# Performance work log

Measured on AMD Instinct MI355X. Metric: run time of the kernel, lower is better.

## Reference

```python
import jax, jax.numpy as jnp
import numpy as np

MODEL_DIM = 1024
NUM_HEADS = 16
K_DIM = MODEL_DIM // NUM_HEADS


def setup_inputs() -> dict:
    key = jax.random.key(0)
    kx, kw1, kw2 = jax.random.split(key, 3)
    B, L, D = 4, 2048, MODEL_DIM
    x = jax.random.normal(kx, (B, L, D), dtype=jnp.float32)
    # nn.Linear(D, 3D, bias=False): y = x @ W^T; store transposed form [D, 3D]
    scale1 = 1.0 / np.sqrt(D)
    Wqkv = jax.random.uniform(kw1, (D, 3 * D), dtype=jnp.float32, minval=-scale1, maxval=scale1)
    Wout = jax.random.uniform(kw2, (D, D), dtype=jnp.float32, minval=-scale1, maxval=scale1)
    return {"x": x, "Wqkv": Wqkv, "Wout": Wout}


def reference(x, Wqkv, Wout):
    B, L, D = x.shape
    H, Kd = NUM_HEADS, K_DIM
    qkv = x @ Wqkv  # [B, L, 3D]
    q, k, v = jnp.split(qkv, 3, axis=-1)

    def heads(t):  # [B, L, D] -> [B, H, L, Kd]
        return t.reshape(B, L, H, Kd).transpose(0, 2, 1, 3)

    qh, kh, vh = heads(q), heads(k), heads(v)
    scores = jnp.einsum('bhqd,bhkd->bhqk', qh, kh) / jnp.sqrt(jnp.float32(Kd))
    causal = jnp.triu(jnp.ones((L, L), dtype=bool), k=1)  # True above diagonal
    scores = jnp.where(causal, -jnp.inf, scores)
    probs = jax.nn.softmax(scores, axis=-1)
    attended = jnp.einsum('bhqk,bhkd->bhqd', probs, vh)
    concatted = attended.transpose(0, 2, 1, 3).reshape(B, L, D)
    # dropout is identity in eval mode
    return concatted @ Wout
```

## Files before the change

kernel.cpp:

```cpp
#include <hip/hip_runtime.h>

typedef unsigned short u16;
typedef unsigned int   u32;
typedef __bf16   bf16x8 __attribute__((ext_vector_type(8)));
typedef float    f32x4  __attribute__((ext_vector_type(4)));
typedef u16      u16x4  __attribute__((ext_vector_type(4)));
typedef u16      u16x8  __attribute__((ext_vector_type(8)));
typedef u32      u32x2  __attribute__((ext_vector_type(2)));
typedef u32      u32x4  __attribute__((ext_vector_type(4)));

#if __has_builtin(__builtin_amdgcn_exp2f)
#define EXP2(x) __builtin_amdgcn_exp2f(x)
#else
#define EXP2(x) exp2f(x)
#endif

__device__ __forceinline__ u16 f2bf(float f) {
    unsigned u = __float_as_uint(f);
    u += 0x7FFFu + ((u >> 16) & 1u);
    return (u16)(u >> 16);
}

__device__ __forceinline__ u32 pack_bf16(float a, float b) {
#if __has_builtin(__builtin_amdgcn_cvt_pk_bf16_f32)
    typedef __bf16 bf16x2 __attribute__((ext_vector_type(2)));
    bf16x2 r = __builtin_amdgcn_cvt_pk_bf16_f32(a, b);
    return __builtin_bit_cast(u32, r);
#else
    return (u32)f2bf(a) | ((u32)f2bf(b) << 16);
#endif
}

__device__ __forceinline__ void async_copy16(const u16* g, u16* l) {
    __builtin_amdgcn_global_load_lds(
        (const __attribute__((address_space(1))) unsigned*)g,
        (__attribute__((address_space(3))) unsigned*)l, 16, 0, 0);
}

__device__ __forceinline__ bf16x8 lds_frag(const u16* p) {
    return *(const bf16x8*)p;
}

__device__ __forceinline__ void permlane32_swap(u32& a, u32& b) {
    asm("v_permlane32_swap_b32 %0, %1" : "+v"(a), "+v"(b));
}
__device__ __forceinline__ void permlane16_swap(u32& a, u32& b) {
    asm("v_permlane16_swap_b32 %0, %1" : "+v"(a), "+v"(b));
}

__global__ __launch_bounds__(256) void prep(const float* __restrict__ x,
                                            const float* __restrict__ Wqkv,
                                            const float* __restrict__ Wout,
                                            u16* __restrict__ xb,
                                            u16* __restrict__ wqkv_t,
                                            u16* __restrict__ wout_t) {
    __shared__ u16 t[64 * 72];
    const int bid = blockIdx.x;
    const int tid = threadIdx.x;

    if (bid >= 1024) {
        size_t i = ((size_t)(bid - 1024) * 256 + tid) * 8;
        float4 v0 = *(const float4*)(x + i);
        float4 v1 = *(const float4*)(x + i + 4);
        u16x8 o = { f2bf(v0.x), f2bf(v0.y), f2bf(v0.z), f2bf(v0.w),
                    f2bf(v1.x), f2bf(v1.y), f2bf(v1.z), f2bf(v1.w) };
        *(u16x8*)(xb + i) = o;
        return;
    }

    const float* W;  u16* Wt;  int Kd, Nd, n0, k0;
    if (bid < 768) { W = Wqkv; Wt = wqkv_t; Kd = 1024; Nd = 3072;
                     n0 = (bid % 48) * 64; k0 = (bid / 48) * 64; }
    else           { W = Wout; Wt = wout_t; Kd = 1024; Nd = 1024;
                     n0 = ((bid - 768) % 16) * 64; k0 = ((bid - 768) / 16) * 64; }
#pragma unroll
    for (int i = 0; i < 4; ++i) {
        int lin = i * 256 + tid;
        int kr = lin >> 4, nc = (lin & 15) << 2;
        float4 v = *(const float4*)(W + (size_t)(k0 + kr) * Nd + n0 + nc);
        u16x4 o = { f2bf(v.x), f2bf(v.y), f2bf(v.z), f2bf(v.w) };
        *(u16x4*)&t[kr * 72 + nc] = o;
    }
    __syncthreads();
#pragma unroll
    for (int i = 0; i < 2; ++i) {
        int lin = i * 256 + tid;
        int nr = lin >> 3, kc = (lin & 7) << 3;
        u16x8 o;
#pragma unroll
        for (int jj = 0; jj < 8; ++jj) o[jj] = t[(kc + jj) * 72 + nr];
        *(u16x8*)(Wt + (size_t)(n0 + nr) * Kd + k0 + kc) = o;
    }
}

__global__ __launch_bounds__(256) void gemm_qkv(const u16* __restrict__ A,
                                                const u16* __restrict__ Bt,
                                                u16* __restrict__ outb,
                                                int K, int N) {
    __shared__ u16 As[2][128 * 32];
    __shared__ u16 Bs[2][128 * 32];
    const int tid = threadIdx.x;
    const int lane = tid & 63;
    const int wv = tid >> 6;
    const int wr = (wv >> 1) * 64;
    const int wc = (wv & 1) * 64;
    const int qd = lane >> 4;
    const int c  = lane & 15;

    const int flat = blockIdx.x;
    const int r_ = flat & 7;
    const int q_ = flat >> 3;
    const int m0 = ((r_ >> 1) * 16 + q_ / 12) * 128;
    const int n0 = ((r_ & 1) * 12 + q_ % 12) * 128;

    const int srow = tid >> 2;
    const int sg = ((tid & 3) ^ ((srow >> 1) & 3)) << 3;

    const u16* Ag0 = A  + (size_t)(m0 +      srow) * K + sg;
    const u16* Ag1 = A  + (size_t)(m0 + 64 + srow) * K + sg;
    const u16* Bg0 = Bt + (size_t)(n0 +      srow) * K + sg;
    const u16* Bg1 = Bt + (size_t)(n0 + 64 + srow) * K + sg;

    const u32 fsw = (qd ^ ((c >> 1) & 3)) << 3;
    const u32 a_off = (wr + c) * 32 + fsw;
    const u32 b_off = (wc + c) * 32 + fsw;

    f32x4 acc[4][4] = {};

    async_copy16(Ag0, &As[0][tid * 8]);
    async_copy16(Ag1, &As[0][2048 + tid * 8]);
    async_copy16(Bg0, &Bs[0][tid * 8]);
    async_copy16(Bg1, &Bs[0][2048 + tid * 8]);

    int p = 0;
    for (int k0 = 0; k0 < K; k0 += 32) {
        __syncthreads();
        if (k0 + 32 < K) {
            const int np = p ^ 1;
            async_copy16(Ag0 + k0 + 32, &As[np][tid * 8]);
            async_copy16(Ag1 + k0 + 32, &As[np][2048 + tid * 8]);
            async_copy16(Bg0 + k0 + 32, &Bs[np][tid * 8]);
            async_copy16(Bg1 + k0 + 32, &Bs[np][2048 + tid * 8]);
        }
        bf16x8 af[4], bfr[4];
#pragma unroll
        for (int i = 0; i < 4; ++i) af[i]  = lds_frag(&As[p][a_off + i * 512]);
#pragma unroll
        for (int j = 0; j < 4; ++j) bfr[j] = lds_frag(&Bs[p][b_off + j * 512]);
#pragma unroll
        for (int i = 0; i < 4; ++i)
#pragma unroll
            for (int j = 0; j < 4; ++j)
                acc[i][j] = __builtin_amdgcn_mfma_f32_16x16x32_bf16(af[i], bfr[j], acc[i][j], 0, 0, 0);
        p ^= 1;
    }

#pragma unroll
    for (int i = 0; i < 4; ++i)
#pragma unroll
        for (int j = 0; j < 4; ++j) {
            int n = n0 + wc + j * 16 + c;
            int which = n >> 10, h = (n >> 6) & 15, kd = n & 63;
            int m_base = m0 + wr + i * 16 + qd * 4;
            int b = m_base >> 11, l0 = m_base & 2047;
            int bh = b * 16 + h;
            if (which == 2) {
                u32x2 o2;
                o2[0] = pack_bf16(acc[i][j][0], acc[i][j][1]);
                o2[1] = pack_bf16(acc[i][j][2], acc[i][j][3]);
                *(u32x2*)(outb + (size_t)(128 + bh) * 131072 + (size_t)kd * 2048 + l0) = o2;
            } else if (which == 0) {
#pragma unroll
                for (int r = 0; r < 4; ++r)
                    outb[(size_t)bh * 131072 + (size_t)(l0 + r) * 64 + kd] =
                        f2bf(acc[i][j][r] * 0.1803368801f);
            } else {
#pragma unroll
                for (int r = 0; r < 4; ++r)
                    outb[(size_t)(64 + bh) * 131072 + (size_t)(l0 + r) * 64 + kd] =
                        f2bf(acc[i][j][r]);
            }
        }
}

__global__ __launch_bounds__(256) void gemm_out(const u16* __restrict__ A,
                                                const u16* __restrict__ Bt,
                                                float* __restrict__ outf,
                                                int K, int N) {
    __shared__ u16 As[2][64 * 32];
    __shared__ u16 Bs[2][128 * 32];
    const int tid = threadIdx.x;
    const int lane = tid & 63;
    const int wv = tid >> 6;
    const int wr = (wv >> 1) * 32;
    const int wc = (wv & 1) * 64;
    const int qd = lane >> 4;
    const int c  = lane & 15;

    const int flat = blockIdx.x + 8 * blockIdx.y;
    const int r_ = flat & 7;
    const int q_ = flat >> 3;
    const int m0 = (r_ * 16 + (q_ >> 3)) * 64;
    const int n0 = (q_ & 7) * 128;

    const int srow = tid >> 2;
    const int sg = ((tid & 3) ^ ((srow >> 1) & 3)) << 3;

    const u16* Ag0 = A  + (size_t)(m0 +      srow) * K + sg;
    const u16* Bg0 = Bt + (size_t)(n0 +      srow) * K + sg;
    const u16* Bg1 = Bt + (size_t)(n0 + 64 + srow) * K + sg;

    const u32 fsw = (qd ^ ((c >> 1) & 3)) << 3;
    const u32 a_off = (wr + c) * 32 + fsw;
    const u32 b_off = (wc + c) * 32 + fsw;

    f32x4 acc[2][4] = {};

    async_copy16(Ag0, &As[0][tid * 8]);
    async_copy16(Bg0, &Bs[0][tid * 8]);
    async_copy16(Bg1, &Bs[0][2048 + tid * 8]);

    int p = 0;
    for (int k0 = 0; k0 < K; k0 += 32) {
        __syncthreads();
        if (k0 + 32 < K) {
            const int np = p ^ 1;
            async_copy16(Ag0 + k0 + 32, &As[np][tid * 8]);
            async_copy16(Bg0 + k0 + 32, &Bs[np][tid * 8]);
            async_copy16(Bg1 + k0 + 32, &Bs[np][2048 + tid * 8]);
        }
        bf16x8 af[2], bfr[4];
#pragma unroll
        for (int i = 0; i < 2; ++i) af[i]  = lds_frag(&As[p][a_off + i * 512]);
#pragma unroll
        for (int j = 0; j < 4; ++j) bfr[j] = lds_frag(&Bs[p][b_off + j * 512]);
#pragma unroll
        for (int i = 0; i < 2; ++i)
#pragma unroll
            for (int j = 0; j < 4; ++j)
                acc[i][j] = __builtin_amdgcn_mfma_f32_16x16x32_bf16(af[i], bfr[j], acc[i][j], 0, 0, 0);
        p ^= 1;
    }

#pragma unroll
    for (int i = 0; i < 2; ++i)
#pragma unroll
        for (int j = 0; j < 4; ++j)
#pragma unroll
            for (int r = 0; r < 4; ++r) {
                int m = m0 + wr + i * 16 + qd * 4 + r;
                int n = n0 + wc + j * 16 + c;
                outf[(size_t)m * N + n] = acc[i][j][r];
            }
}

#define ATTN_S_AB(KSB)                                                        \
    do {                                                                      \
        _Pragma("unroll") for (int f = 0; f < 8; ++f) {                       \
            sa[f] = f32x4{-8.f, -8.f, -8.f, -8.f};                            \
            sb[f] = f32x4{-8.f, -8.f, -8.f, -8.f};                            \
        }                                                                     \
        __builtin_amdgcn_s_setprio(1);                                        \
        _Pragma("unroll") for (int ks = 0; ks < 2; ++ks) {                    \
            const u16* kp = (KSB) + kf_off[ks];                               \
            _Pragma("unroll") for (int f = 0; f < 8; ++f) {                   \
                bf16x8 kf = lds_frag(kp + f * 1024);                          \
                sa[f] = __builtin_amdgcn_mfma_f32_16x16x32_bf16(              \
                    kf, qa[ks], sa[f], 0, 0, 0);                              \
                sb[f] = __builtin_amdgcn_mfma_f32_16x16x32_bf16(              \
                    kf, qb[ks], sb[f], 0, 0, 0);                              \
            }                                                                 \
        }                                                                     \
        __builtin_amdgcn_s_setprio(0);                                        \
    } while (0)

#define ATTN_FINISH_AB(VTB, KT)                                               \
    do {                                                                      \
        if ((KT) == qt) {                                                     \
            _Pragma("unroll") for (int f = 0; f < 8; ++f)                     \
                _Pragma("unroll") for (int r = 0; r < 4; ++r) {               \
                    int key = (KT) * 128 + f * 16 + qd * 4 + r;               \
                    if (key > qa_row) sa[f][r] = -3e38f;                      \
                    if (key > qb_row) sb[f][r] = -3e38f;                      \
                }                                                             \
        }                                                                     \
        _Pragma("unroll") for (int f = 0; f < 8; ++f) {                       \
            _Pragma("unroll") for (int r = 0; r < 4; ++r) {                   \
                sa[f][r] = EXP2(sa[f][r]);                                    \
                sb[f][r] = EXP2(sb[f][r]);                                    \
            }                                                                 \
            rva += sa[f];                                                     \
            rvb += sb[f];                                                     \
        }                                                                     \
        _Pragma("unroll") for (int kc = 0; kc < 4; ++kc) {                    \
            u32 a0 = pack_bf16(sa[2 * kc][0], sa[2 * kc][1]);                 \
            u32 a1 = pack_bf16(sa[2 * kc + 1][0], sa[2 * kc + 1][1]);         \
            u32 b0 = pack_bf16(sa[2 * kc][2], sa[2 * kc][3]);                 \
            u32 b1 = pack_bf16(sa[2 * kc + 1][2], sa[2 * kc + 1][3]);         \
            permlane32_swap(a0, a1); permlane16_swap(a0, a1);                 \
            permlane32_swap(b0, b1); permlane16_swap(b0, b1);                 \
            u32x4 wpa = {a0, b0, a1, b1};                                     \
            bf16x8 pa = __builtin_bit_cast(bf16x8, wpa);                      \
            u32 c0 = pack_bf16(sb[2 * kc][0], sb[2 * kc][1]);                 \
            u32 c1 = pack_bf16(sb[2 * kc + 1][0], sb[2 * kc + 1][1]);         \
            u32 d0 = pack_bf16(sb[2 * kc][2], sb[2 * kc][3]);                 \
            u32 d1 = pack_bf16(sb[2 * kc + 1][2], sb[2 * kc + 1][3]);         \
            permlane32_swap(c0, c1); permlane16_swap(c0, c1);                 \
            permlane32_swap(d0, d1); permlane16_swap(d0, d1);                 \
            u32x4 wpb = {c0, d0, c1, d1};                                     \
            bf16x8 pb = __builtin_bit_cast(bf16x8, wpb);                      \
            const u16* vp = (VTB) + vf_off[kc];                               \
            __builtin_amdgcn_s_setprio(1);                                    \
            _Pragma("unroll") for (int jo = 0; jo < 4; ++jo) {                \
                bf16x8 vf = lds_frag(vp + jo * 2048);                         \
                acca[jo] = __builtin_amdgcn_mfma_f32_16x16x32_bf16(           \
                    vf, pa, acca[jo], 0, 0, 0);                               \
                accb[jo] = __builtin_amdgcn_mfma_f32_16x16x32_bf16(           \
                    vf, pb, accb[jo], 0, 0, 0);                               \
            }                                                                 \
            __builtin_amdgcn_s_setprio(0);                                    \
        }                                                                     \
    } while (0)

__global__ __launch_bounds__(256, 2) void attn_kernel(const u16* __restrict__ qkv,
                                                      u16* __restrict__ att) {
    __shared__ u16 Ks[2][128 * 64];
    __shared__ u16 Vt[2][64 * 128];

    const int tid = threadIdx.x;
    const int lane = tid & 63;
    const int w = tid >> 6;
    const int qd = lane >> 4;
    const int c = lane & 15;

    const int flat = blockIdx.x + 8 * blockIdx.y;
    const int bh = (flat & 7) + 8 * ((flat >> 3) & 7);
    const int bx = flat >> 6;
    const int b = bh >> 4, h = bh & 15;

    const u16* Qg = qkv + (size_t)bh * 131072;
    const u16* Kg = qkv + (size_t)(64 + bh) * 131072;
    const u16* Vg = qkv + (size_t)(128 + bh) * 131072;

    u32 kf_off[2];
#pragma unroll
    for (int ks = 0; ks < 2; ++ks)
        kf_off[ks] = c * 64 + (((ks * 4 + qd) ^ (c & 7)) << 3);
    u32 vf_off[4];
#pragma unroll
    for (int kc = 0; kc < 4; ++kc)
        vf_off[kc] = c * 128 + (((kc * 4 + qd) ^ c) << 3);

    auto issue_copy = [&](int t, u16* kd, u16* vd) {
#pragma unroll
        for (int it = 0; it < 4; ++it) {
            int lin = it * 256 + tid;
            int krw = lin >> 3, kch = lin & 7;
            int vrw = lin >> 4, vch = lin & 15;
            async_copy16(Kg + (size_t)t * 8192 + krw * 64 + ((kch ^ (krw & 7)) << 3),
                         kd + lin * 8);
            async_copy16(Vg + (size_t)t * 128 + (size_t)vrw * 2048 + ((vch ^ (vrw & 15)) << 3),
                         vd + lin * 8);
        }
    };

#pragma unroll 1
    for (int seg = 0; seg < 2; ++seg) {
        const int qt = seg ? (15 - bx) : bx;
        const int qa_row = qt * 128 + w * 32 + c;
        const int qb_row = qa_row + 16;

        bf16x8 qa[2], qb[2];
#pragma unroll
        for (int ks = 0; ks < 2; ++ks) {
            qa[ks] = *(const bf16x8*)(Qg + (size_t)qa_row * 64 + ks * 32 + qd * 8);
            qb[ks] = *(const bf16x8*)(Qg + (size_t)qb_row * 64 + ks * 32 + qd * 8);
        }

        f32x4 acca[4] = {}, accb[4] = {};
        f32x4 rva = {}, rvb = {};
        f32x4 sa[8], sb[8];

        const int nkt = qt + 1;

        __syncthreads();
        issue_copy(0, Ks[0], Vt[0]);
        __syncthreads();
        if (nkt > 1) issue_copy(1, Ks[1], Vt[1]);

#pragma unroll 1
        for (int kt = 0; kt < nkt; ++kt) {
            const int p = kt & 1;
            ATTN_S_AB(Ks[p]);
            ATTN_FINISH_AB(Vt[p], kt);
            if (kt + 1 < nkt) {
                __syncthreads();
                if (kt + 2 < nkt) issue_copy(kt + 2, Ks[p], Vt[p]);
            }
        }

        float ra = rva[0] + rva[1] + rva[2] + rva[3];
        float rb = rvb[0] + rvb[1] + rvb[2] + rvb[3];
        ra += __shfl_xor(ra, 16, 64);
        ra += __shfl_xor(ra, 32, 64);
        rb += __shfl_xor(rb, 16, 64);
        rb += __shfl_xor(rb, 32, 64);
        float ia = __builtin_amdgcn_rcpf(ra), ib = __builtin_amdgcn_rcpf(rb);
        u16* ar = att + ((size_t)b * 2048 + qa_row) * 1024 + h * 64;
        u16* br = att + ((size_t)b * 2048 + qb_row) * 1024 + h * 64;
#pragma unroll
        for (int jo = 0; jo < 4; ++jo) {
            u32x2 oa, ob;
            oa[0] = pack_bf16(acca[jo][0] * ia, acca[jo][1] * ia);
            oa[1] = pack_bf16(acca[jo][2] * ia, acca[jo][3] * ia);
            ob[0] = pack_bf16(accb[jo][0] * ib, accb[jo][1] * ib);
            ob[1] = pack_bf16(accb[jo][2] * ib, accb[jo][3] * ib);
            *(u32x2*)(ar + jo * 16 + qd * 4) = oa;
            *(u32x2*)(br + jo * 16 + qd * 4) = ob;
        }
    }
}

extern "C" void kernel_launch(void* const* d_in, const int* in_sizes, int n_in,
                              void* d_out, int out_size, void* d_ws, size_t ws_size,
                              hipStream_t stream) {
    const float* x    = (const float*)d_in[0];
    const float* Wqkv = (const float*)d_in[1];
    const float* Wout = (const float*)d_in[2];
    float* out = (float*)d_out;

    char* ws = (char*)d_ws;
    u16* x_bf   = (u16*)(ws);
    u16* wqkv_t = (u16*)(ws + 16777216);
    u16* wout_t = (u16*)(ws + 23068672);
    u16* qkv_h  = (u16*)(ws + 25165824);
    u16* att    = (u16*)(ws + 75497472);

    prep<<<dim3(5120), dim3(256), 0, stream>>>(x, Wqkv, Wout, x_bf, wqkv_t, wout_t);
    gemm_qkv<<<dim3(1536), dim3(256), 0, stream>>>(x_bf, wqkv_t, qkv_h, 1024, 3072);
    attn_kernel<<<dim3(8, 64), dim3(256), 0, stream>>>(qkv_h, att);
    gemm_out<<<dim3(8, 128), dim3(256), 0, stream>>>(att, wout_t, out, 1024, 1024);
}
```

Measured before the change: 242.5 us.

## Software-pipeline attention: compute next tile's QK scores before current tile's PV

Restructures the attention inner loop so the QK^T score MFMAs for key tile kt+1 are issued before the softmax/PV stage of tile kt, using two alternating score register sets. V tiles move to a triple-buffered LDS ring so the next copy can overwrite a V buffer no longer in use while the current one is still being read. The aim is to overlap exp/pack/permlane work with MFMA issue. In exchange it doubles score-register pressure under launch_bounds(256,2), which risks spills or lower occupancy, and adds one extra 16KB V buffer in LDS.

```diff
diff --git a/kernel.cpp b/kernel.cpp
--- a/kernel.cpp
+++ b/kernel.cpp
@@ -254,57 +254,57 @@
             }
 }
 
-#define ATTN_S_AB(KSB)                                                        \
+#define ATTN_S_SET(KSB, SA, SB)                                               \
     do {                                                                      \
         _Pragma("unroll") for (int f = 0; f < 8; ++f) {                       \
-            sa[f] = f32x4{-8.f, -8.f, -8.f, -8.f};                            \
-            sb[f] = f32x4{-8.f, -8.f, -8.f, -8.f};                            \
+            SA[f] = f32x4{-8.f, -8.f, -8.f, -8.f};                            \
+            SB[f] = f32x4{-8.f, -8.f, -8.f, -8.f};                            \
         }                                                                     \
         __builtin_amdgcn_s_setprio(1);                                        \
         _Pragma("unroll") for (int ks = 0; ks < 2; ++ks) {                    \
             const u16* kp = (KSB) + kf_off[ks];                               \
             _Pragma("unroll") for (int f = 0; f < 8; ++f) {                   \
                 bf16x8 kf = lds_frag(kp + f * 1024);                          \
-                sa[f] = __builtin_amdgcn_mfma_f32_16x16x32_bf16(              \
-                    kf, qa[ks], sa[f], 0, 0, 0);                              \
-                sb[f] = __builtin_amdgcn_mfma_f32_16x16x32_bf16(              \
-                    kf, qb[ks], sb[f], 0, 0, 0);                              \
+                SA[f] = __builtin_amdgcn_mfma_f32_16x16x32_bf16(              \
+                    kf, qa[ks], SA[f], 0, 0, 0);                              \
+                SB[f] = __builtin_amdgcn_mfma_f32_16x16x32_bf16(              \
+                    kf, qb[ks], SB[f], 0, 0, 0);                              \
             }                                                                 \
         }                                                                     \
         __builtin_amdgcn_s_setprio(0);                                        \
     } while (0)
 
-#define ATTN_FINISH_AB(VTB, KT)                                               \
+#define ATTN_FINISH_SET(VTB, KT, SA, SB)                                      \
     do {                                                                      \
         if ((KT) == qt) {                                                     \
             _Pragma("unroll") for (int f = 0; f < 8; ++f)                     \
                 _Pragma("unroll") for (int r = 0; r < 4; ++r) {               \
                     int key = (KT) * 128 + f * 16 + qd * 4 + r;               \
-                    if (key > qa_row) sa[f][r] = -3e38f;                      \
-                    if (key > qb_row) sb[f][r] = -3e38f;                      \
+                    if (key > qa_row) SA[f][r] = -3e38f;                      \
+                    if (key > qb_row) SB[f][r] = -3e38f;                      \
                 }                                                             \
         }                                                                     \
         _Pragma("unroll") for (int f = 0; f < 8; ++f) {                       \
             _Pragma("unroll") for (int r = 0; r < 4; ++r) {                   \
-                sa[f][r] = EXP2(sa[f][r]);                                    \
-                sb[f][r] = EXP2(sb[f][r]);                                    \
+                SA[f][r] = EXP2(SA[f][r]);                                    \
+                SB[f][r] = EXP2(SB[f][r]);                                    \
             }                                                                 \
-            rva += sa[f];                                                     \
-            rvb += sb[f];                                                     \
+            rva += SA[f];                                                     \
+            rvb += SB[f];                                                     \
         }                                                                     \
         _Pragma("unroll") for (int kc = 0; kc < 4; ++kc) {                    \
-            u32 a0 = pack_bf16(sa[2 * kc][0], sa[2 * kc][1]);                 \
-            u32 a1 = pack_bf16(sa[2 * kc + 1][0], sa[2 * kc + 1][1]);         \
-            u32 b0 = pack_bf16(sa[2 * kc][2], sa[2 * kc][3]);                 \
-            u32 b1 = pack_bf16(sa[2 * kc + 1][2], sa[2 * kc + 1][3]);         \
+            u32 a0 = pack_bf16(SA[2 * kc][0], SA[2 * kc][1]);                 \
+            u32 a1 = pack_bf16(SA[2 * kc + 1][0], SA[2 * kc + 1][1]);         \
+            u32 b0 = pack_bf16(SA[2 * kc][2], SA[2 * kc][3]);                 \
+            u32 b1 = pack_bf16(SA[2 * kc + 1][2], SA[2 * kc + 1][3]);         \
             permlane32_swap(a0, a1); permlane16_swap(a0, a1);                 \
             permlane32_swap(b0, b1); permlane16_swap(b0, b1);                 \
             u32x4 wpa = {a0, b0, a1, b1};                                     \
             bf16x8 pa = __builtin_bit_cast(bf16x8, wpa);                      \
-            u32 c0 = pack_bf16(sb[2 * kc][0], sb[2 * kc][1]);                 \
-            u32 c1 = pack_bf16(sb[2 * kc + 1][0], sb[2 * kc + 1][1]);         \
-            u32 d0 = pack_bf16(sb[2 * kc][2], sb[2 * kc][3]);                 \
-            u32 d1 = pack_bf16(sb[2 * kc + 1][2], sb[2 * kc + 1][3]);         \
+            u32 c0 = pack_bf16(SB[2 * kc][0], SB[2 * kc][1]);                 \
+            u32 c1 = pack_bf16(SB[2 * kc + 1][0], SB[2 * kc + 1][1]);         \
+            u32 d0 = pack_bf16(SB[2 * kc][2], SB[2 * kc][3]);                 \
+            u32 d1 = pack_bf16(SB[2 * kc + 1][2], SB[2 * kc + 1][3]);         \
             permlane32_swap(c0, c1); permlane16_swap(c0, c1);                 \
             permlane32_swap(d0, d1); permlane16_swap(d0, d1);                 \
             u32x4 wpb = {c0, d0, c1, d1};                                     \
@@ -325,7 +325,7 @@
 __global__ __launch_bounds__(256, 2) void attn_kernel(const u16* __restrict__ qkv,
                                                       u16* __restrict__ att) {
     __shared__ u16 Ks[2][128 * 64];
-    __shared__ u16 Vt[2][64 * 128];
+    __shared__ u16 Vt[3][64 * 128];
 
     const int tid = threadIdx.x;
     const int lane = tid & 63;
@@ -379,7 +379,7 @@
 
         f32x4 acca[4] = {}, accb[4] = {};
         f32x4 rva = {}, rvb = {};
-        f32x4 sa[8], sb[8];
+        f32x4 saA[8], sbA[8], saB[8], sbB[8];
 
         const int nkt = qt + 1;
 
@@ -387,16 +387,28 @@
         issue_copy(0, Ks[0], Vt[0]);
         __syncthreads();
         if (nkt > 1) issue_copy(1, Ks[1], Vt[1]);
+        ATTN_S_SET(Ks[0], saA, sbA);
+
+        u16 *vPV = Vt[0], *vNx = Vt[1], *vFr = Vt[2];
 
 #pragma unroll 1
         for (int kt = 0; kt < nkt; ++kt) {
-            const int p = kt & 1;
-            ATTN_S_AB(Ks[p]);
-            ATTN_FINISH_AB(Vt[p], kt);
-            if (kt + 1 < nkt) {
-                __syncthreads();
-                if (kt + 2 < nkt) issue_copy(kt + 2, Ks[p], Vt[p]);
+            if ((kt & 1) == 0) {
+                if (kt + 1 < nkt) {
+                    __syncthreads();
+                    if (kt + 2 < nkt) issue_copy(kt + 2, Ks[kt & 1], vFr);
+                    ATTN_S_SET(Ks[(kt + 1) & 1], saB, sbB);
+                }
+                ATTN_FINISH_SET(vPV, kt, saA, sbA);
+            } else {
+                if (kt + 1 < nkt) {
+                    __syncthreads();
+                    if (kt + 2 < nkt) issue_copy(kt + 2, Ks[kt & 1], vFr);
+                    ATTN_S_SET(Ks[(kt + 1) & 1], saA, sbA);
+                }
+                ATTN_FINISH_SET(vPV, kt, saB, sbB);
             }
+            u16* t0 = vPV; vPV = vNx; vNx = vFr; vFr = t0;
         }
 
         float ra = rva[0] + rva[1] + rva[2] + rva[3];
```

Result: slower. 686.1 us (+182.9%).
